# Performance work log

Hardware: AMD Instinct MI355X
Metric: run time of the kernel (lower is better)

## Reference

```python
import jax, jax.numpy as jnp
import numpy as np

N_NODES = 100000
N_EDGES = 1200000
IN_DIM = 64
OUT_DIM = 64
LN_EPS = 1e-5


def setup_inputs() -> dict:
    key = jax.random.key(0)
    k_x, k_e, k_w, k_b, k_g, k_beta = jax.random.split(key, 6)
    x = jax.random.normal(k_x, (N_NODES, IN_DIM), dtype=jnp.float32)
    edge_index = jax.random.randint(k_e, (2, N_EDGES), 0, N_NODES, dtype=jnp.int64)
    # nn.Linear(in_dim*2, out_dim): weight [out, 2*in], bias [out]
    lim = 1.0 / np.sqrt(2 * IN_DIM)
    W = jax.random.uniform(k_w, (OUT_DIM, 2 * IN_DIM), minval=-lim, maxval=lim, dtype=jnp.float32)
    b = jax.random.uniform(k_b, (OUT_DIM,), minval=-lim, maxval=lim, dtype=jnp.float32)
    gamma = jnp.ones((OUT_DIM,), dtype=jnp.float32)
    beta = jnp.zeros((OUT_DIM,), dtype=jnp.float32)
    return {"x": x, "W": W, "b": b, "gamma": gamma, "beta": beta, "edge_index": edge_index}


def reference(x, W, b, gamma, beta, edge_index):
    i = edge_index[0]  # destination nodes (aggregation target)
    j = edge_index[1]  # source nodes (neighbor features)
    n = x.shape[0]
    # mean aggregation: scatter-add gathered neighbor feats, divide by degree
    agg = jax.ops.segment_sum(x[j], i, num_segments=n)  # [N, in_dim]
    deg = jax.ops.segment_sum(jnp.ones(i.shape, x.dtype), i, num_segments=n)
    agg = agg / jnp.maximum(deg, 1.0)[:, None]
    # concat + linear + relu
    h = jnp.concatenate([x, agg], axis=-1) @ W.T + b  # [N, out_dim]
    h = jax.nn.relu(h)
    # layernorm (dropout p=0 is identity in eval)
    mu = jnp.mean(h, axis=-1, keepdims=True)
    var = jnp.var(h, axis=-1, keepdims=True)
    return (h - mu) / jnp.sqrt(var + LN_EPS) * gamma + beta
```

## Files before the change

kernel.cpp:

```cpp
#include <hip/hip_runtime.h>
#include <hip/hip_bf16.h>

#define N_NODES 100000
#define N_EDGES 1200000
#define LN_EPS 1e-5f
#define CAP 40
#define NBIN 782
#define BINW 128
#define BCAP 1792
#define EPB 4096
#define P1_BLOCKS 293
#define CONV_BLOCKS 507
#define NSTRIDE 42

typedef __attribute__((ext_vector_type(8))) short short8;
typedef __attribute__((ext_vector_type(4))) float float4v;
typedef __attribute__((ext_vector_type(2))) int   ivec2;

__device__ __forceinline__ short bfb(float v) {
    __hip_bfloat16 h = __float2bfloat16(v);
    short s; __builtin_memcpy(&s, &h, 2); return s;
}
__device__ __forceinline__ float b2f(unsigned short u) {
    unsigned int xi = ((unsigned int)u) << 16;
    float f; __builtin_memcpy(&f, &xi, 4); return f;
}

__global__ __launch_bounds__(256) void k_bin3(
    const float* __restrict__ x, unsigned short* __restrict__ xb,
    const int* __restrict__ ei, int* __restrict__ btail,
    int* __restrict__ binbuf)
{
    const int tid = threadIdx.x;

    if (blockIdx.x >= P1_BLOCKS) {
        for (int i = (blockIdx.x - P1_BLOCKS) * 256 + tid; i < N_NODES * 8;
             i += CONV_BLOCKS * 256) {
            float4v f0 = *(const float4v*)(x + 8 * i);
            float4v f1 = *(const float4v*)(x + 8 * i + 4);
            short8 p;
            p[0] = bfb(f0.x); p[1] = bfb(f0.y); p[2] = bfb(f0.z); p[3] = bfb(f0.w);
            p[4] = bfb(f1.x); p[5] = bfb(f1.y); p[6] = bfb(f1.z); p[7] = bfb(f1.w);
            *(short8*)(xb + 8 * i) = p;
        }
        return;
    }

    __shared__ int   bcnt[NBIN];
    __shared__ int   bbase[NBIN];
    __shared__ int   bgbase[NBIN];
    __shared__ int   bfill[NBIN];
    __shared__ int   scanbuf[256];
    __shared__ ivec2 stage[EPB];

    for (int i = tid; i < NBIN; i += 256) { bcnt[i] = 0; bfill[i] = 0; }
    __syncthreads();

    const int ebase = blockIdx.x * EPB;
    int d[16], s[16];
#pragma unroll
    for (int u = 0; u < 16; ++u) {
        int e = ebase + u * 256 + tid;
        bool v = (e < N_EDGES);
        d[u] = v ? ei[e] : -1;
        s[u] = v ? ei[N_EDGES + e] : 0;
        if (v) atomicAdd(&bcnt[d[u] >> 7], 1);
    }
    __syncthreads();

    int v4[4], tsum = 0;
#pragma unroll
    for (int k = 0; k < 4; ++k) {
        int b = 4 * tid + k;
        v4[k] = (b < NBIN) ? bcnt[b] : 0;
        tsum += v4[k];
    }
    scanbuf[tid] = tsum;
    __syncthreads();
    for (int off = 1; off < 256; off <<= 1) {
        int t = (tid >= off) ? scanbuf[tid - off] : 0;
        __syncthreads();
        scanbuf[tid] += t;
        __syncthreads();
    }
    int run = scanbuf[tid] - tsum;
#pragma unroll
    for (int k = 0; k < 4; ++k) {
        int b = 4 * tid + k;
        if (b < NBIN) bbase[b] = run;
        run += v4[k];
    }
    const int tot = scanbuf[255];

    for (int b = tid; b < NBIN; b += 256) {
        int c = bcnt[b];
        bgbase[b] = c ? atomicAdd(&btail[b], c) : 0;
    }
    __syncthreads();

#pragma unroll
    for (int u = 0; u < 16; ++u) {
        if (d[u] >= 0) {
            int b = d[u] >> 7;
            int p = bbase[b] + atomicAdd(&bfill[b], 1);
            stage[p] = (ivec2){d[u], s[u]};
        }
    }
    __syncthreads();

    for (int i = tid; i < tot; i += 256) {
        ivec2 e = stage[i];
        int b = e.x >> 7;
        int pos = bgbase[b] + (i - bbase[b]);
        if (pos < BCAP)
            binbuf[(size_t)b * BCAP + pos] = ((e.x & 127) << 17) | e.y;
    }
}

__global__ __launch_bounds__(512) void node_fused(
    const unsigned short* __restrict__ xb,
    const int* __restrict__ btail, const int* __restrict__ binbuf,
    const float* __restrict__ W, const float* __restrict__ bias,
    const float* __restrict__ gamma, const float* __restrict__ beta,
    float* __restrict__ out)
{
    __shared__ short Wl[64 * 136];
    __shared__ int   nlist[BINW * NSTRIDE];
    __shared__ int   lcnt[BINW];

    const int tid = threadIdx.x;
    const int bin = blockIdx.x;
    const int nodebase = bin * BINW;

    for (int i = tid; i < 64 * 64; i += 512) {
        int row = i >> 6, cp = i & 63;
        const float* wr = W + row * 128 + cp * 2;
        short2 v; v.x = bfb(wr[0]); v.y = bfb(wr[1]);
        *(short2*)&Wl[row * 136 + cp * 2] = v;
    }
    for (int i = tid; i < BINW; i += 512) lcnt[i] = 0;
    __syncthreads();

    const int nb = min(btail[bin], BCAP);
    for (int i = tid; i < nb; i += 512) {
        int pk = binbuf[(size_t)bin * BCAP + i];
        int nl = pk >> 17;
        int slot = atomicAdd(&lcnt[nl], 1);
        if (slot < CAP) nlist[nl * NSTRIDE + slot] = pk & 0x1FFFF;
    }
    __syncthreads();

    const int wid  = tid >> 6;
    const int lane = tid & 63;
    const int g    = lane >> 4;
    const int c    = lane & 15;
    const int nbase = nodebase + wid * 16;
    if (nbase >= N_NODES) return;

    float bs_[4], gm_[4], bt_[4];
#pragma unroll
    for (int ct = 0; ct < 4; ++ct) {
        bs_[ct] = bias[ct * 16 + c];
        gm_[ct] = gamma[ct * 16 + c];
        bt_[ct] = beta[ct * 16 + c];
    }

    const unsigned short* xrow = xb + (nbase + c) * 64 + g * 8;
    short8 A0 = *(const short8*)(xrow);
    short8 A1 = *(const short8*)(xrow + 32);

    int dfull[4], dgs[4];
#pragma unroll
    for (int r = 0; r < 4; ++r) {
        dfull[r] = lcnt[wid * 16 + r * 4 + g];
        dgs[r]   = min(dfull[r], CAP);
    }
    float4v a[4];
#pragma unroll
    for (int r = 0; r < 4; ++r) a[r] = (float4v){0.f, 0.f, 0.f, 0.f};

    const int dmax = max(max(dgs[0], dgs[1]), max(dgs[2], dgs[3]));
    for (int t = 0; t < dmax; t += 4) {
        int j[16];
#pragma unroll
        for (int r = 0; r < 4; ++r) {
            const int* ip = &nlist[(wid * 16 + r * 4 + g) * NSTRIDE + t];
            ivec2 p0 = *(const ivec2*)ip;
            ivec2 p1 = *(const ivec2*)(ip + 2);
            j[4 * r + 0] = p0.x; j[4 * r + 1] = p0.y;
            j[4 * r + 2] = p1.x; j[4 * r + 3] = p1.y;
        }
#pragma unroll
        for (int r = 0; r < 4; ++r) {
#pragma unroll
            for (int u = 0; u < 4; ++u) {
                if (t + u < dgs[r]) {
                    ushort4 v = *(const ushort4*)(xb + j[4 * r + u] * 64 + c * 4);
                    a[r].x += b2f(v.x); a[r].y += b2f(v.y);
                    a[r].z += b2f(v.z); a[r].w += b2f(v.w);
                }
            }
        }
    }

    short* aL = (short*)&nlist[wid * 16 * NSTRIDE];
#pragma unroll
    for (int r = 0; r < 4; ++r) {
        float rd = 1.0f / fmaxf((float)dfull[r], 1.0f);
        int m = r * 4 + g;
        short sa = bfb(a[r].x * rd), sb = bfb(a[r].y * rd),
              sc = bfb(a[r].z * rd), sd = bfb(a[r].w * rd);
        int lo = (int)(unsigned short)sa | ((int)(unsigned short)sb << 16);
        int hi = (int)(unsigned short)sc | ((int)(unsigned short)sd << 16);
        *(ivec2*)(aL + m * 72 + c * 4) = (ivec2){lo, hi};
    }
    short8 A2 = *(const short8*)(aL + c * 72 + g * 8);
    short8 A3 = *(const short8*)(aL + c * 72 + 32 + g * 8);

    float4v acc[4];
#pragma unroll
    for (int ct = 0; ct < 4; ++ct) {
        float bb = bs_[ct];
        acc[ct] = (float4v){bb, bb, bb, bb};
    }
#pragma unroll
    for (int ks = 0; ks < 4; ++ks) {
        short8 Af = (ks == 0) ? A0 : (ks == 1) ? A1 : (ks == 2) ? A2 : A3;
#pragma unroll
        for (int ct = 0; ct < 4; ++ct) {
            short8 Bf = *(const short8*)(Wl + (ct * 16 + c) * 136 + ks * 32 + g * 8);
            acc[ct] = __builtin_amdgcn_mfma_f32_16x16x32_bf16(Af, Bf, acc[ct], 0, 0, 0);
        }
    }

    float s_[4] = {0, 0, 0, 0}, q_[4] = {0, 0, 0, 0};
#pragma unroll
    for (int ct = 0; ct < 4; ++ct)
#pragma unroll
        for (int r = 0; r < 4; ++r) {
            float h = fmaxf(acc[ct][r], 0.0f);
            acc[ct][r] = h;
            s_[r] += h;
            q_[r] += h * h;
        }
#pragma unroll
    for (int off = 1; off <= 8; off <<= 1)
#pragma unroll
        for (int r = 0; r < 4; ++r) {
            s_[r] += __shfl_xor(s_[r], off);
            q_[r] += __shfl_xor(q_[r], off);
        }
#pragma unroll
    for (int r = 0; r < 4; ++r) {
        float mu = s_[r] * (1.0f / 64.0f);
        float var = q_[r] * (1.0f / 64.0f) - mu * mu;
        float is = rsqrtf(var + LN_EPS);
        int node = nbase + g * 4 + r;
        if (node < N_NODES) {
#pragma unroll
            for (int ct = 0; ct < 4; ++ct) {
                out[node * 64 + ct * 16 + c] =
                    (acc[ct][r] - mu) * is * gm_[ct] + bt_[ct];
            }
        }
    }
}

extern "C" void kernel_launch(void* const* d_in, const int* in_sizes, int n_in,
                              void* d_out, int out_size, void* d_ws, size_t ws_size,
                              hipStream_t stream) {
    const float* x     = (const float*)d_in[0];
    const float* W     = (const float*)d_in[1];
    const float* b     = (const float*)d_in[2];
    const float* gamma = (const float*)d_in[3];
    const float* beta  = (const float*)d_in[4];
    const int*   ei    = (const int*)d_in[5];
    float* out = (float*)d_out;

    int* btail = (int*)d_ws;
    int* binbuf = (int*)((char*)d_ws + 4096);
    unsigned short* xb = (unsigned short*)(binbuf + (size_t)NBIN * BCAP);

    (void)hipMemsetAsync(btail, 0, NBIN * sizeof(int), stream);

    k_bin3<<<P1_BLOCKS + CONV_BLOCKS, 256, 0, stream>>>(x, xb, ei, btail, binbuf);
    node_fused<<<NBIN, 512, 0, stream>>>(xb, btail, binbuf, W, b, gamma, beta, out);
}
```

Baseline: 167.2 us.

## Split node bins across two 256-thread blocks and widen gather loads to 16 bytes

Each 128-node bin is now handled by two 64-node blocks of 256 threads. Both blocks scan the full bin edge list and keep only the edges whose destination falls in their half. The neighbour gather now has each lane load 8 bf16 values (16 bytes) per edge, with two lanes splitting the edges of a node and combining their sums through a cross-lane shuffle. The goal is more blocks for occupancy and wider memory transactions. The cost is that every bin's edge list is read twice and the W tile is converted twice as often.

New measurement: 150.9 us. 1.11x faster.

```diff
diff --git a/kernel.cpp b/kernel.cpp
--- a/kernel.cpp
+++ b/kernel.cpp
@@ -12,8 +12,10 @@
 #define P1_BLOCKS 293
 #define CONV_BLOCKS 507
 #define NSTRIDE 42
+#define NBLK2 1563
 
 typedef __attribute__((ext_vector_type(8))) short short8;
+typedef __attribute__((ext_vector_type(8))) unsigned short us8;
 typedef __attribute__((ext_vector_type(4))) float float4v;
 typedef __attribute__((ext_vector_type(2))) int   ivec2;
 
@@ -117,7 +119,7 @@
     }
 }
 
-__global__ __launch_bounds__(512) void node_fused(
+__global__ __launch_bounds__(256, 4) void node_fused(
     const unsigned short* __restrict__ xb,
     const int* __restrict__ btail, const int* __restrict__ binbuf,
     const float* __restrict__ W, const float* __restrict__ bias,
@@ -125,28 +127,31 @@
     float* __restrict__ out)
 {
     __shared__ short Wl[64 * 136];
-    __shared__ int   nlist[BINW * NSTRIDE];
-    __shared__ int   lcnt[BINW];
+    __shared__ int   nlist[64 * NSTRIDE];
+    __shared__ int   lcnt[64];
 
     const int tid = threadIdx.x;
-    const int bin = blockIdx.x;
-    const int nodebase = bin * BINW;
-
-    for (int i = tid; i < 64 * 64; i += 512) {
+    const int bin  = blockIdx.x >> 1;
+    const int half = blockIdx.x & 1;
+    const int nodebase = blockIdx.x * 64;
+
+    for (int i = tid; i < 64 * 64; i += 256) {
         int row = i >> 6, cp = i & 63;
         const float* wr = W + row * 128 + cp * 2;
         short2 v; v.x = bfb(wr[0]); v.y = bfb(wr[1]);
         *(short2*)&Wl[row * 136 + cp * 2] = v;
     }
-    for (int i = tid; i < BINW; i += 512) lcnt[i] = 0;
+    if (tid < 64) lcnt[tid] = 0;
     __syncthreads();
 
     const int nb = min(btail[bin], BCAP);
-    for (int i = tid; i < nb; i += 512) {
+    for (int i = tid; i < nb; i += 256) {
         int pk = binbuf[(size_t)bin * BCAP + i];
-        int nl = pk >> 17;
-        int slot = atomicAdd(&lcnt[nl], 1);
-        if (slot < CAP) nlist[nl * NSTRIDE + slot] = pk & 0x1FFFF;
+        int nl = (pk >> 17) - (half << 6);
+        if ((unsigned)nl < 64u) {
+            int slot = atomicAdd(&lcnt[nl], 1);
+            if (slot < CAP) nlist[nl * NSTRIDE + slot] = pk & 0x1FFFF;
+        }
     }
     __syncthreads();
 
@@ -154,8 +159,62 @@
     const int lane = tid & 63;
     const int g    = lane >> 4;
     const int c    = lane & 15;
+    const int ch   = c & 7;
+    const int pr   = c >> 3;
     const int nbase = nodebase + wid * 16;
     if (nbase >= N_NODES) return;
+
+    int dfull[4], dgs[4];
+#pragma unroll
+    for (int r = 0; r < 4; ++r) {
+        dfull[r] = lcnt[wid * 16 + r * 4 + g];
+        dgs[r]   = min(dfull[r], CAP);
+    }
+    float aa[4][8];
+#pragma unroll
+    for (int r = 0; r < 4; ++r)
+#pragma unroll
+        for (int k = 0; k < 8; ++k) aa[r][k] = 0.0f;
+
+    const int dmax = max(max(dgs[0], dgs[1]), max(dgs[2], dgs[3]));
+    for (int t = 0; t < dmax; t += 8) {
+#pragma unroll
+        for (int u = 0; u < 4; ++u) {
+#pragma unroll
+            for (int r = 0; r < 4; ++r) {
+                int idx = t + 2 * u + pr;
+                if (idx < dgs[r]) {
+                    int j = nlist[(wid * 16 + r * 4 + g) * NSTRIDE + idx];
+                    us8 v = *(const us8*)(xb + (size_t)j * 64 + ch * 8);
+#pragma unroll
+                    for (int k = 0; k < 8; ++k) aa[r][k] += b2f(v[k]);
+                }
+            }
+        }
+    }
+
+    const unsigned short* xrow = xb + (size_t)(nbase + c) * 64 + g * 8;
+    short8 A0 = *(const short8*)(xrow);
+    short8 A1 = *(const short8*)(xrow + 32);
+
+#pragma unroll
+    for (int r = 0; r < 4; ++r)
+#pragma unroll
+        for (int k = 0; k < 8; ++k) aa[r][k] += __shfl_xor(aa[r][k], 8);
+
+    short* aL = (short*)&nlist[wid * 16 * NSTRIDE];
+#pragma unroll
+    for (int r = 0; r < 4; ++r) {
+        float rd = 1.0f / fmaxf((float)dfull[r], 1.0f);
+        int m = r * 4 + g;
+        short8 p;
+#pragma unroll
+        for (int k = 0; k < 8; ++k) p[k] = bfb(aa[r][k] * rd);
+        if (pr == 0)
+            *(short8*)(aL + m * 72 + ch * 8) = p;
+    }
+    short8 A2 = *(const short8*)(aL + c * 72 + g * 8);
+    short8 A3 = *(const short8*)(aL + c * 72 + 32 + g * 8);
 
     float bs_[4], gm_[4], bt_[4];
 #pragma unroll
@@ -164,58 +223,6 @@
         gm_[ct] = gamma[ct * 16 + c];
         bt_[ct] = beta[ct * 16 + c];
     }
-
-    const unsigned short* xrow = xb + (nbase + c) * 64 + g * 8;
-    short8 A0 = *(const short8*)(xrow);
-    short8 A1 = *(const short8*)(xrow + 32);
-
-    int dfull[4], dgs[4];
-#pragma unroll
-    for (int r = 0; r < 4; ++r) {
-        dfull[r] = lcnt[wid * 16 + r * 4 + g];
-        dgs[r]   = min(dfull[r], CAP);
-    }
-    float4v a[4];
-#pragma unroll
-    for (int r = 0; r < 4; ++r) a[r] = (float4v){0.f, 0.f, 0.f, 0.f};
-
-    const int dmax = max(max(dgs[0], dgs[1]), max(dgs[2], dgs[3]));
-    for (int t = 0; t < dmax; t += 4) {
-        int j[16];
-#pragma unroll
-        for (int r = 0; r < 4; ++r) {
-            const int* ip = &nlist[(wid * 16 + r * 4 + g) * NSTRIDE + t];
-            ivec2 p0 = *(const ivec2*)ip;
-            ivec2 p1 = *(const ivec2*)(ip + 2);
-            j[4 * r + 0] = p0.x; j[4 * r + 1] = p0.y;
-            j[4 * r + 2] = p1.x; j[4 * r + 3] = p1.y;
-        }
-#pragma unroll
-        for (int r = 0; r < 4; ++r) {
-#pragma unroll
-            for (int u = 0; u < 4; ++u) {
-                if (t + u < dgs[r]) {
-                    ushort4 v = *(const ushort4*)(xb + j[4 * r + u] * 64 + c * 4);
-                    a[r].x += b2f(v.x); a[r].y += b2f(v.y);
-                    a[r].z += b2f(v.z); a[r].w += b2f(v.w);
-                }
-            }
-        }
-    }
-
-    short* aL = (short*)&nlist[wid * 16 * NSTRIDE];
-#pragma unroll
-    for (int r = 0; r < 4; ++r) {
-        float rd = 1.0f / fmaxf((float)dfull[r], 1.0f);
-        int m = r * 4 + g;
-        short sa = bfb(a[r].x * rd), sb = bfb(a[r].y * rd),
-              sc = bfb(a[r].z * rd), sd = bfb(a[r].w * rd);
-        int lo = (int)(unsigned short)sa | ((int)(unsigned short)sb << 16);
-        int hi = (int)(unsigned short)sc | ((int)(unsigned short)sd << 16);
-        *(ivec2*)(aL + m * 72 + c * 4) = (ivec2){lo, hi};
-    }
-    short8 A2 = *(const short8*)(aL + c * 72 + g * 8);
-    short8 A3 = *(const short8*)(aL + c * 72 + 32 + g * 8);
 
     float4v acc[4];
 #pragma unroll
@@ -284,5 +291,5 @@
     (void)hipMemsetAsync(btail, 0, NBIN * sizeof(int), stream);
 
     k_bin3<<<P1_BLOCKS + CONV_BLOCKS, 256, 0, stream>>>(x, xb, ei, btail, binbuf);
-    node_fused<<<NBIN, 512, 0, stream>>>(xb, btail, binbuf, W, b, gamma, beta, out);
-}
+    node_fused<<<NBLK2, 256, 0, stream>>>(xb, btail, binbuf, W, b, gamma, beta, out);
+}
```
